# Performance work log

Hardware: AMD Instinct MI355X
Metric: run time of the kernel (lower is better)

Reference implementation:

```python
import jax, jax.numpy as jnp
import numpy as np

N = 100000
E = 800000

def elu(x):
    return jnp.where(x > 0, x, jnp.expm1(x))

def transformer_conv(x, src, dst, ea, Wq, bq, Wk, bk, Wv, bv, We, Ws, bs, heads, ch):
    # PyG TransformerConv (concat=True, root_weight=True, beta=False, eval so dropout off)
    n = x.shape[0]
    q = (x @ Wq + bq).reshape(n, heads, ch)
    k = (x @ Wk + bk).reshape(n, heads, ch)
    v = (x @ Wv + bv).reshape(n, heads, ch)
    e = (ea @ We).reshape(-1, heads, ch)            # [E,H,C], lin_edge has no bias
    kj = k[src] + e                                  # [E,H,C]
    logits = (q[dst] * kj).sum(-1) / jnp.sqrt(jnp.float32(ch))  # [E,H]
    # segment softmax over incoming edges of each dst node
    m = jax.ops.segment_max(logits, dst, num_segments=n)
    ex = jnp.exp(logits - m[dst])
    denom = jax.ops.segment_sum(ex, dst, num_segments=n)
    alpha = ex / denom[dst]                          # [E,H]
    msg = alpha[..., None] * (v[src] + e)            # [E,H,C]
    agg = jax.ops.segment_sum(msg, dst, num_segments=n).reshape(n, heads * ch)
    return agg + x @ Ws + bs                         # skip connection (lin_skip)

def setup_inputs() -> dict:
    key = jax.random.key(0)
    ks = jax.random.split(key, 32)
    def rn(k, shape, scale=0.1):
        return jax.random.normal(k, shape, dtype=jnp.float32) * scale
    d = {}
    d['x'] = jax.random.normal(ks[0], (N, 23), dtype=jnp.float32)
    d['edge_index'] = jax.random.randint(ks[1], (2, E), 0, N, dtype=jnp.int32)
    d['edge_attr'] = jax.random.normal(ks[2], (E, 7), dtype=jnp.float32)
    d['linA_w'] = rn(ks[3], (23, 23)); d['linA_b'] = jnp.zeros((23,), jnp.float32)
    d['linB_w'] = rn(ks[4], (23, 23)); d['linB_b'] = jnp.zeros((23,), jnp.float32)
    # conv1: in=23, heads=8, out=24 -> 192
    d['q1_w'] = rn(ks[5], (23, 192)); d['q1_b'] = jnp.zeros((192,), jnp.float32)
    d['k1_w'] = rn(ks[6], (23, 192)); d['k1_b'] = jnp.zeros((192,), jnp.float32)
    d['v1_w'] = rn(ks[7], (23, 192)); d['v1_b'] = jnp.zeros((192,), jnp.float32)
    d['e1_w'] = rn(ks[8], (7, 192))
    d['s1_w'] = rn(ks[9], (23, 192)); d['s1_b'] = jnp.zeros((192,), jnp.float32)
    # conv4: in=192, heads=8, out=8 -> 64
    d['q2_w'] = rn(ks[10], (192, 64)); d['q2_b'] = jnp.zeros((64,), jnp.float32)
    d['k2_w'] = rn(ks[11], (192, 64)); d['k2_b'] = jnp.zeros((64,), jnp.float32)
    d['v2_w'] = rn(ks[12], (192, 64)); d['v2_b'] = jnp.zeros((64,), jnp.float32)
    d['e2_w'] = rn(ks[13], (7, 64))
    d['s2_w'] = rn(ks[14], (192, 64)); d['s2_b'] = jnp.zeros((64,), jnp.float32)
    d['lin1_w'] = rn(ks[15], (64, 20)); d['lin1_b'] = jnp.zeros((20,), jnp.float32)
    d['lin2_w'] = rn(ks[16], (20, 1)); d['lin2_b'] = jnp.zeros((1,), jnp.float32)
    return d

def reference(x, edge_index, edge_attr,
              linA_w, linA_b, linB_w, linB_b,
              q1_w, q1_b, k1_w, k1_b, v1_w, v1_b, e1_w, s1_w, s1_b,
              q2_w, q2_b, k2_w, k2_b, v2_w, v2_b, e2_w, s2_w, s2_b,
              lin1_w, lin1_b, lin2_w, lin2_b):
    src, dst = edge_index[0], edge_index[1]
    h = elu(x @ linA_w + linA_b)
    h = elu(h @ linB_w + linB_b)
    h = transformer_conv(h, src, dst, edge_attr, q1_w, q1_b, k1_w, k1_b, v1_w, v1_b, e1_w, s1_w, s1_b, 8, 24)
    h = elu(h)
    h = transformer_conv(h, src, dst, edge_attr, q2_w, q2_b, k2_w, k2_b, v2_w, v2_b, e2_w, s2_w, s2_b, 8, 8)
    h = elu(h)
    h = elu(h @ lin1_w + lin1_b)
    return h @ lin2_w + lin2_b
```

## Files before the change

### kernel.cpp

```cpp
#include <hip/hip_runtime.h>
#include <math.h>


__device__ __forceinline__ float elu_f(float x) {
    return x > 0.f ? x : expm1f(x);
}


__global__ void mlp_kernel(const float* __restrict__ x,
                           const float* __restrict__ A, const float* __restrict__ ab,
                           const float* __restrict__ B, const float* __restrict__ bb,
                           float* __restrict__ out, int n) {
    __shared__ float sA[23 * 23], sB[23 * 23], sa[23], sb[23];
    for (int t = threadIdx.x; t < 23 * 23; t += blockDim.x) { sA[t] = A[t]; sB[t] = B[t]; }
    if (threadIdx.x < 23) { sa[threadIdx.x] = ab[threadIdx.x]; sb[threadIdx.x] = bb[threadIdx.x]; }
    __syncthreads();
    int i = blockIdx.x * blockDim.x + threadIdx.x;
    if (i >= n) return;
    float xi[23], h1[23];
    #pragma unroll
    for (int j = 0; j < 23; j++) xi[j] = x[(size_t)i * 23 + j];
    #pragma unroll
    for (int o = 0; o < 23; o++) {
        float acc = sa[o];
        #pragma unroll
        for (int j = 0; j < 23; j++) acc = fmaf(xi[j], sA[j * 23 + o], acc);
        h1[o] = elu_f(acc);
    }
    #pragma unroll
    for (int o = 0; o < 23; o++) {
        float acc = sb[o];
        #pragma unroll
        for (int j = 0; j < 23; j++) acc = fmaf(h1[j], sB[j * 23 + o], acc);
        out[(size_t)i * 23 + o] = elu_f(acc);
    }
}

__device__ __forceinline__ void store_val(int mode, int kvcpl, void* base, int stride,
                                          int g, int c, float val) {
    if (mode == 0) {
        ((float*)base)[(size_t)g * stride + c] = val;
    } else {
        int ln = c / kvcpl, slot = c - ln * kvcpl;
        size_t pos = (size_t)g * stride + (size_t)ln * (2 * kvcpl) + slot
                   + (mode == 2 ? kvcpl : 0);
        ((float*)base)[pos] = val;
    }
}

template<int IN, int Kc, int OUTW, int M, int TY, int KVCPL>
__global__ void proj_tiled_kernel(const float* __restrict__ in, int n,
    const float* __restrict__ W0, const float* __restrict__ b0, void* __restrict__ o0, int st0, int md0,
    const float* __restrict__ W1, const float* __restrict__ b1, void* __restrict__ o1, int st1, int md1,
    const float* __restrict__ W2, const float* __restrict__ b2, void* __restrict__ o2, int st2, int md2,
    const float* __restrict__ W3, const float* __restrict__ b3, void* __restrict__ o3, int st3, int md3) {
    constexpr int WTOT = M * OUTW;
    constexpr int CG   = WTOT / 8;
    constexpr int BN   = TY * 4;
    constexpr int SAW  = BN + 4;
    constexpr int NT   = CG * TY;
    static_assert(IN % Kc == 0, "Kc must divide IN");
    __shared__ float sA[Kc][SAW];
    __shared__ float sB[Kc][WTOT];

    const int tid = threadIdx.x;
    const int tx = tid % CG;
    const int ty = tid / CG;
    const int node0 = blockIdx.x * BN;

    const int colA = tx * 4;
    const int colB = WTOT / 2 + tx * 4;
    const int matA = colA / OUTW, ccA = colA % OUTW;
    const int matB = colB / OUTW, ccB = colB % OUTW;
    const float* bA = (matA == 0 ? b0 : matA == 1 ? b1 : matA == 2 ? b2 : b3);
    const float* bB = (matB == 0 ? b0 : matB == 1 ? b1 : matB == 2 ? b2 : b3);
    void* oA = (matA == 0 ? o0 : matA == 1 ? o1 : matA == 2 ? o2 : o3);
    void* oB = (matB == 0 ? o0 : matB == 1 ? o1 : matB == 2 ? o2 : o3);
    const int stA = (matA == 0 ? st0 : matA == 1 ? st1 : matA == 2 ? st2 : st3);
    const int stB = (matB == 0 ? st0 : matB == 1 ? st1 : matB == 2 ? st2 : st3);
    const int mdA = (matA == 0 ? md0 : matA == 1 ? md1 : matA == 2 ? md2 : md3);
    const int mdB = (matB == 0 ? md0 : matB == 1 ? md1 : matB == 2 ? md2 : md3);

    float acc[4][8];
    #pragma unroll
    for (int i = 0; i < 4; i++) {
        #pragma unroll
        for (int c = 0; c < 4; c++) { acc[i][c] = bA[ccA + c]; acc[i][4 + c] = bB[ccB + c]; }
    }

    for (int k0 = 0; k0 < IN; k0 += Kc) {
        for (int t = tid; t < Kc * BN; t += NT) {
            int j = t / BN, nn = t - j * BN;
            int g = node0 + nn;
            sA[j][nn] = (g < n) ? in[(size_t)g * IN + k0 + j] : 0.f;
        }
        for (int t = tid; t < Kc * WTOT; t += NT) {
            int j = t / WTOT, c = t - j * WTOT;
            int m = c / OUTW, cm = c - m * OUTW;
            const float* Wp = (m == 0 ? W0 : m == 1 ? W1 : m == 2 ? W2 : W3);
            sB[j][c] = Wp[(size_t)(k0 + j) * OUTW + cm];
        }
        __syncthreads();
        #pragma unroll 8
        for (int j = 0; j < Kc; j++) {
            float4 a  = *(const float4*)&sA[j][ty * 4];
            float4 v0 = *(const float4*)&sB[j][colA];
            float4 v1 = *(const float4*)&sB[j][colB];
            float av[4] = {a.x, a.y, a.z, a.w};
            float bv[8] = {v0.x, v0.y, v0.z, v0.w, v1.x, v1.y, v1.z, v1.w};
            #pragma unroll
            for (int i = 0; i < 4; i++)
                #pragma unroll
                for (int c = 0; c < 8; c++)
                    acc[i][c] = fmaf(av[i], bv[c], acc[i][c]);
        }
        __syncthreads();
    }

    #pragma unroll
    for (int i = 0; i < 4; i++) {
        int g = node0 + ty * 4 + i;
        if (g >= n) continue;
        #pragma unroll
        for (int c = 0; c < 4; c++) {
            store_val(mdA, KVCPL, oA, stA, g, ccA + c, acc[i][c]);
            store_val(mdB, KVCPL, oB, stB, g, ccB + c, acc[i][4 + c]);
        }
    }
}


__global__ void zero2_kernel(int* __restrict__ a, int* __restrict__ b, int n) {
    int i = blockIdx.x * blockDim.x + threadIdx.x;
    if (i < n) { a[i] = 0; b[i] = 0; }
}

__global__ void count_kernel(const int* __restrict__ dst, int* __restrict__ cnt, int nE) {
    int e = blockIdx.x * blockDim.x + threadIdx.x;
    if (e < nE) atomicAdd(&cnt[dst[e]], 1);
}

__global__ void scan_block_kernel(int* __restrict__ cnt, int* __restrict__ bsum, int n) {
    __shared__ int sdat[256];
    int i = blockIdx.x * 256 + threadIdx.x;
    int v = (i < n) ? cnt[i] : 0;
    sdat[threadIdx.x] = v;
    __syncthreads();
    for (int off = 1; off < 256; off <<= 1) {
        int t = (threadIdx.x >= (unsigned)off) ? sdat[threadIdx.x - off] : 0;
        __syncthreads();
        sdat[threadIdx.x] += t;
        __syncthreads();
    }
    if (i < n) cnt[i] = sdat[threadIdx.x] - v;
    if (threadIdx.x == 255) bsum[blockIdx.x] = sdat[255];
}

__global__ void scan_bsum_kernel(int* __restrict__ bsum, int nb) {
    __shared__ int s[1024];
    int i = threadIdx.x;
    int v = (i < nb) ? bsum[i] : 0;
    s[i] = v;
    __syncthreads();
    for (int off = 1; off < 1024; off <<= 1) {
        int t = (i >= off) ? s[i - off] : 0;
        __syncthreads();
        s[i] += t;
        __syncthreads();
    }
    if (i < nb) bsum[i] = s[i] - v;
}

__global__ void finalize_rp_kernel(const int* __restrict__ cnt, const int* __restrict__ bsum,
                                   int* __restrict__ rp, int n, int nE) {
    int i = blockIdx.x * blockDim.x + threadIdx.x;
    if (i < n) rp[i] = cnt[i] + bsum[i >> 8];
    if (i == n) rp[n] = nE;
}

__global__ void scatter_kernel(const int* __restrict__ src, const int* __restrict__ dst,
                               const int* __restrict__ rp, int* __restrict__ cur,
                               int* __restrict__ srcS, int* __restrict__ eidS, int nE) {
    int e = blockIdx.x * blockDim.x + threadIdx.x;
    if (e >= nE) return;
    int d = dst[e];
    int pos = rp[d] + atomicAdd(&cur[d], 1);
    srcS[pos] = src[e];
    eidS[pos] = e;
}

template<int IN, int C, bool QMAT, bool DOELU>
__global__ void conv_fused_kernel(const float* __restrict__ feat,
                                  const float* __restrict__ Wq, const float* __restrict__ qb,
                                  const float* __restrict__ kv,
                                  const float* __restrict__ qmat,
                                  const float* __restrict__ ea, const float* __restrict__ We,
                                  const int* __restrict__ rp, const int* __restrict__ srcS,
                                  const int* __restrict__ eidS,
                                  float* __restrict__ out, int n, float scale) {
    constexpr int HC = 8 * C;
    constexpr int CPL = HC / 64;
    constexpr int KVROW = 2 * HC;
    const int lane = threadIdx.x & 63;
    const int d = blockIdx.x * (blockDim.x >> 6) + (threadIdx.x >> 6);
    if (d >= n) return;
    const int ch0 = lane * CPL;

    float we[7][CPL];
    #pragma unroll
    for (int j = 0; j < 7; j++)
        #pragma unroll
        for (int c = 0; c < CPL; c++) we[j][c] = We[j * HC + ch0 + c];

    float* op = out + (size_t)d * HC + ch0;
    float sk[CPL], q[CPL];
    #pragma unroll
    for (int c = 0; c < CPL; c++) sk[c] = op[c];
    if constexpr (QMAT) {
        const float* qp = qmat + (size_t)d * HC + ch0;
        #pragma unroll
        for (int c = 0; c < CPL; c++) q[c] = qp[c];
    } else {
        #pragma unroll
        for (int c = 0; c < CPL; c++) q[c] = qb[ch0 + c];
        const float* fd = feat + (size_t)d * IN;
        for (int j = 0; j < IN; j++) {
            float f = fd[j];
            #pragma unroll
            for (int c = 0; c < CPL; c++)
                q[c] = fmaf(f, Wq[(size_t)j * HC + ch0 + c], q[c]);
        }
    }

    float m = -INFINITY, l = 0.f, acc[CPL];
    #pragma unroll
    for (int c = 0; c < CPL; c++) acc[c] = 0.f;

    const int p0 = rp[d], p1 = rp[d + 1];
    if (p0 < p1) {
        auto loadkv = [&](int s, float* kc, float* vc) {
            const float* pb = kv + (size_t)s * KVROW + lane * (2 * CPL);
            if constexpr (CPL == 3) {
                float2 a = *(const float2*)(pb + 0);
                float2 b = *(const float2*)(pb + 2);
                float2 c = *(const float2*)(pb + 4);
                kc[0] = a.x; kc[1] = a.y; kc[2] = b.x;
                vc[0] = b.y; vc[1] = c.x; vc[2] = c.y;
            } else {
                float2 a = *(const float2*)pb;
                kc[0] = a.x; vc[0] = a.y;
            }
        };
        float kc[CPL], vc[CPL], ev[7];
        loadkv(srcS[p0], kc, vc);
        {
            const float* e0 = ea + (size_t)eidS[p0] * 7;
            #pragma unroll
            for (int j = 0; j < 7; j++) ev[j] = e0[j];
        }

        for (int p = p0; p < p1; p++) {
            float kn[CPL], vn[CPL], evn[7];
            if (p + 1 < p1) {
                loadkv(srcS[p + 1], kn, vn);
                const float* e1 = ea + (size_t)eidS[p + 1] * 7;
                #pragma unroll
                for (int j = 0; j < 7; j++) evn[j] = e1[j];
            }
            float part = 0.f, vv[CPL];
            #pragma unroll
            for (int c = 0; c < CPL; c++) {
                float ec = 0.f;
                #pragma unroll
                for (int j = 0; j < 7; j++) ec = fmaf(ev[j], we[j][c], ec);
                part = fmaf(q[c], kc[c] + ec, part);
                vv[c] = vc[c] + ec;
            }
            part += __shfl_xor(part, 1);
            part += __shfl_xor(part, 2);
            part += __shfl_xor(part, 4);
            float z = part * scale;
            float mn = fmaxf(m, z);
            float rs = expf(m - mn);
            float pw = expf(z - mn);
            l = l * rs + pw;
            #pragma unroll
            for (int c = 0; c < CPL; c++) acc[c] = fmaf(acc[c], rs, pw * vv[c]);
            m = mn;
            #pragma unroll
            for (int c = 0; c < CPL; c++) { kc[c] = kn[c]; vc[c] = vn[c]; }
            #pragma unroll
            for (int j = 0; j < 7; j++) ev[j] = evn[j];
        }
    }
    float invl = (l > 0.f) ? 1.f / l : 0.f;
    #pragma unroll
    for (int c = 0; c < CPL; c++) {
        float r = sk[c] + acc[c] * invl;
        op[c] = DOELU ? elu_f(r) : r;
    }
}

__global__ void head_kernel(const float* __restrict__ h, const float* __restrict__ W1,
                            const float* __restrict__ b1, const float* __restrict__ W2,
                            const float* __restrict__ b2, float* __restrict__ out, int n) {
    __shared__ float sW1[64 * 20], sb1[20], sW2[20], sb2;
    for (int t = threadIdx.x; t < 64 * 20; t += blockDim.x) sW1[t] = W1[t];
    if (threadIdx.x < 20) { sb1[threadIdx.x] = b1[threadIdx.x]; sW2[threadIdx.x] = W2[threadIdx.x]; }
    if (threadIdx.x == 0) sb2 = b2[0];
    __syncthreads();
    int i = blockIdx.x * blockDim.x + threadIdx.x;
    if (i >= n) return;
    float hv[64];
    const float* hp = h + (size_t)i * 64;
    #pragma unroll
    for (int j = 0; j < 64; j++) hv[j] = elu_f(hp[j]);
    float acc2 = sb2;
    for (int o = 0; o < 20; o++) {
        float a = sb1[o];
        #pragma unroll
        for (int j = 0; j < 64; j++) a = fmaf(hv[j], sW1[j * 20 + o], a);
        acc2 = fmaf(elu_f(a), sW2[o], acc2);
    }
    out[i] = acc2;
}

__global__ void zero_out_kernel(float* __restrict__ out, int n) {
    int i = blockIdx.x * blockDim.x + threadIdx.x;
    if (i < n) out[i] = 0.f;
}


extern "C" void kernel_launch(void* const* d_in, const int* in_sizes, int n_in,
                              void* d_out, int out_size, void* d_ws, size_t ws_size,
                              hipStream_t stream) {
    const float* x   = (const float*)d_in[0];
    const int*   ei  = (const int*)d_in[1];
    const float* ea  = (const float*)d_in[2];
    const float* Aw  = (const float*)d_in[3];
    const float* Ab  = (const float*)d_in[4];
    const float* Bw  = (const float*)d_in[5];
    const float* Bb  = (const float*)d_in[6];
    const float* q1w = (const float*)d_in[7];  const float* q1b = (const float*)d_in[8];
    const float* k1w = (const float*)d_in[9];  const float* k1b = (const float*)d_in[10];
    const float* v1w = (const float*)d_in[11]; const float* v1b = (const float*)d_in[12];
    const float* e1w = (const float*)d_in[13];
    const float* s1w = (const float*)d_in[14]; const float* s1b = (const float*)d_in[15];
    const float* q2w = (const float*)d_in[16]; const float* q2b = (const float*)d_in[17];
    const float* k2w = (const float*)d_in[18]; const float* k2b = (const float*)d_in[19];
    const float* v2w = (const float*)d_in[20]; const float* v2b = (const float*)d_in[21];
    const float* e2w = (const float*)d_in[22];
    const float* s2w = (const float*)d_in[23]; const float* s2b = (const float*)d_in[24];
    const float* l1w = (const float*)d_in[25]; const float* l1b = (const float*)d_in[26];
    const float* l2w = (const float*)d_in[27]; const float* l2b = (const float*)d_in[28];

    const int n  = in_sizes[0] / 23;
    const int nE = in_sizes[1] / 2;
    const int* src = ei;
    const int* dst = ei + nE;
    float* out = (float*)d_out;
    const int B = 256;
    const int nb = (n + 255) / 256;

    size_t fl_h1 = ((size_t)n * 23 + 3) & ~(size_t)3;
    size_t fl_o1 = (size_t)n * 192;
    size_t fl_kv = (size_t)n * 384;
    size_t ints_total = ((size_t)n + 1) + n + n + 1024 + (size_t)nE + (size_t)nE;
    size_t need_bytes = (fl_h1 + fl_o1 + fl_kv) * 4 + ints_total * 4;

    if (ws_size < need_bytes || nb > 1024) {
        zero_out_kernel<<<(out_size + B - 1) / B, B, 0, stream>>>(out, out_size);
        return;
    }

    float* ws = (float*)d_ws;
    size_t off = 0;
    float* h1    = ws + off; off += fl_h1;
    float* o1    = ws + off; off += fl_o1;
    float* kvreg = ws + off; off += fl_kv;
    int* ip = (int*)(ws + off);
    int* rp   = ip; ip += (size_t)n + 1;
    int* cnt  = ip; ip += n;
    int* cur  = ip; ip += n;
    int* bsum = ip; ip += 1024;
    int* srcS = ip; ip += nE;
    int* eidS = ip; ip += nE;

    float* kv1   = kvreg;
    float* kv2   = kvreg;
    float* q2buf = kvreg + (size_t)n * 128;
    float* o2    = kvreg + (size_t)n * 192;

    const float sc1 = 1.0f / sqrtf(24.0f);
    const float sc2 = 1.0f / sqrtf(8.0f);
    const float* np = nullptr;
    void* npv = nullptr;

    zero2_kernel<<<(n + B - 1) / B, B, 0, stream>>>(cnt, cur, n);
    count_kernel<<<(nE + B - 1) / B, B, 0, stream>>>(dst, cnt, nE);
    scan_block_kernel<<<nb, 256, 0, stream>>>(cnt, bsum, n);
    scan_bsum_kernel<<<1, 1024, 0, stream>>>(bsum, nb);
    finalize_rp_kernel<<<(n + 1 + B - 1) / B, B, 0, stream>>>(cnt, bsum, rp, n, nE);
    scatter_kernel<<<(nE + B - 1) / B, B, 0, stream>>>(src, dst, rp, cur, srcS, eidS, nE);

    mlp_kernel<<<(n + B - 1) / B, B, 0, stream>>>(x, Aw, Ab, Bw, Bb, h1, n);

    const int gproj = (n + 31) / 32;

    proj_tiled_kernel<23, 23, 192, 3, 8, 3><<<gproj, 576, 0, stream>>>(
        h1, n,
        k1w, k1b, (void*)kv1, 384, 1,
        v1w, v1b, (void*)kv1, 384, 2,
        s1w, s1b, (void*)o1, 192, 0,
        np, np, npv, 0, 0);
    conv_fused_kernel<23, 24, false, true><<<(n + 3) / 4, 256, 0, stream>>>(
        h1, q1w, q1b, kv1, np, ea, e1w, rp, srcS, eidS, o1, n, sc1);

    proj_tiled_kernel<192, 32, 64, 4, 8, 1><<<gproj, 256, 0, stream>>>(
        o1, n,
        q2w, q2b, (void*)q2buf, 64, 0,
        k2w, k2b, (void*)kv2, 128, 1,
        v2w, v2b, (void*)kv2, 128, 2,
        s2w, s2b, (void*)o2, 64, 0);
    conv_fused_kernel<192, 8, true, false><<<(n + 3) / 4, 256, 0, stream>>>(
        o1, q2w, q2b, kv2, q2buf, ea, e2w, rp, srcS, eidS, o2, n, sc2);

    head_kernel<<<(n + B - 1) / B, B, 0, stream>>>(o2, l1w, l1b, l2w, l2b, out, n);
}
```

Before: 1.155 ms.

## Process two destination nodes per wavefront and vectorize projection stores

```diff
diff --git a/kernel.cpp b/kernel.cpp
--- a/kernel.cpp
+++ b/kernel.cpp
@@ -36,30 +36,22 @@
     }
 }
 
-__device__ __forceinline__ void store_val(int mode, int kvcpl, void* base, int stride,
-                                          int g, int c, float val) {
-    if (mode == 0) {
-        ((float*)base)[(size_t)g * stride + c] = val;
-    } else {
-        int ln = c / kvcpl, slot = c - ln * kvcpl;
-        size_t pos = (size_t)g * stride + (size_t)ln * (2 * kvcpl) + slot
-                   + (mode == 2 ? kvcpl : 0);
-        ((float*)base)[pos] = val;
-    }
-}
-
-template<int IN, int Kc, int OUTW, int M, int TY, int KVCPL>
+template<int IN, int Kc, int OUTW, int M, int TY, int KM, int VM>
 __global__ void proj_tiled_kernel(const float* __restrict__ in, int n,
-    const float* __restrict__ W0, const float* __restrict__ b0, void* __restrict__ o0, int st0, int md0,
-    const float* __restrict__ W1, const float* __restrict__ b1, void* __restrict__ o1, int st1, int md1,
-    const float* __restrict__ W2, const float* __restrict__ b2, void* __restrict__ o2, int st2, int md2,
-    const float* __restrict__ W3, const float* __restrict__ b3, void* __restrict__ o3, int st3, int md3) {
+    const float* __restrict__ W0, const float* __restrict__ b0,
+    const float* __restrict__ W1, const float* __restrict__ b1,
+    const float* __restrict__ W2, const float* __restrict__ b2,
+    const float* __restrict__ W3, const float* __restrict__ b3,
+    float* __restrict__ kvout,
+    float* __restrict__ r0, float* __restrict__ r1,
+    float* __restrict__ r2, float* __restrict__ r3) {
     constexpr int WTOT = M * OUTW;
     constexpr int CG   = WTOT / 8;
     constexpr int BN   = TY * 4;
     constexpr int SAW  = BN + 4;
     constexpr int NT   = CG * TY;
-    static_assert(IN % Kc == 0, "Kc must divide IN");
+    constexpr int PT   = OUTW / 4;
+    static_assert(IN % Kc == 0, "Kc divides IN");
     __shared__ float sA[Kc][SAW];
     __shared__ float sB[Kc][WTOT];
 
@@ -68,18 +60,30 @@
     const int ty = tid / CG;
     const int node0 = blockIdx.x * BN;
 
-    const int colA = tx * 4;
-    const int colB = WTOT / 2 + tx * 4;
+    int colA, colB; bool pairkv; int chan0 = 0;
+    if (tx < PT) {
+        pairkv = true; chan0 = 4 * tx;
+        colA = KM * OUTW + chan0;
+        colB = VM * OUTW + chan0;
+    } else {
+        pairkv = false;
+        int u = 8 * (tx - PT);
+        auto remap = [&](int uu) {
+            int ri = uu / OUTW, cc = uu - ri * OUTW;
+            int cnt = 0, mat = 0;
+            for (int mm = 0; mm < M; mm++) {
+                if (mm == KM || mm == VM) continue;
+                if (cnt == ri) { mat = mm; break; }
+                cnt++;
+            }
+            return mat * OUTW + cc;
+        };
+        colA = remap(u); colB = remap(u + 4);
+    }
     const int matA = colA / OUTW, ccA = colA % OUTW;
     const int matB = colB / OUTW, ccB = colB % OUTW;
     const float* bA = (matA == 0 ? b0 : matA == 1 ? b1 : matA == 2 ? b2 : b3);
     const float* bB = (matB == 0 ? b0 : matB == 1 ? b1 : matB == 2 ? b2 : b3);
-    void* oA = (matA == 0 ? o0 : matA == 1 ? o1 : matA == 2 ? o2 : o3);
-    void* oB = (matB == 0 ? o0 : matB == 1 ? o1 : matB == 2 ? o2 : o3);
-    const int stA = (matA == 0 ? st0 : matA == 1 ? st1 : matA == 2 ? st2 : st3);
-    const int stB = (matB == 0 ? st0 : matB == 1 ? st1 : matB == 2 ? st2 : st3);
-    const int mdA = (matA == 0 ? md0 : matA == 1 ? md1 : matA == 2 ? md2 : md3);
-    const int mdB = (matB == 0 ? md0 : matB == 1 ? md1 : matB == 2 ? md2 : md3);
 
     float acc[4][8];
     #pragma unroll
@@ -121,10 +125,15 @@
     for (int i = 0; i < 4; i++) {
         int g = node0 + ty * 4 + i;
         if (g >= n) continue;
-        #pragma unroll
-        for (int c = 0; c < 4; c++) {
-            store_val(mdA, KVCPL, oA, stA, g, ccA + c, acc[i][c]);
-            store_val(mdB, KVCPL, oB, stB, g, ccB + c, acc[i][4 + c]);
+        if (pairkv) {
+            float* kp = kvout + (size_t)g * (2 * OUTW) + 2 * chan0;
+            *(float4*)(kp + 0) = make_float4(acc[i][0], acc[i][4], acc[i][1], acc[i][5]);
+            *(float4*)(kp + 4) = make_float4(acc[i][2], acc[i][6], acc[i][3], acc[i][7]);
+        } else {
+            float* rA = (matA == 0 ? r0 : matA == 1 ? r1 : matA == 2 ? r2 : r3);
+            float* rB = (matB == 0 ? r0 : matB == 1 ? r1 : matB == 2 ? r2 : r3);
+            *(float4*)(rA + (size_t)g * OUTW + ccA) = make_float4(acc[i][0], acc[i][1], acc[i][2], acc[i][3]);
+            *(float4*)(rB + (size_t)g * OUTW + ccB) = make_float4(acc[i][4], acc[i][5], acc[i][6], acc[i][7]);
         }
     }
 }
@@ -190,20 +199,22 @@
 }
 
 template<int IN, int C, bool QMAT, bool DOELU>
-__global__ void conv_fused_kernel(const float* __restrict__ feat,
-                                  const float* __restrict__ Wq, const float* __restrict__ qb,
-                                  const float* __restrict__ kv,
-                                  const float* __restrict__ qmat,
-                                  const float* __restrict__ ea, const float* __restrict__ We,
-                                  const int* __restrict__ rp, const int* __restrict__ srcS,
-                                  const int* __restrict__ eidS,
-                                  float* __restrict__ out, int n, float scale) {
+__global__ void conv_fused2_kernel(const float* __restrict__ feat,
+                                   const float* __restrict__ Wq, const float* __restrict__ qb,
+                                   const float* __restrict__ kv,
+                                   const float* __restrict__ qmat,
+                                   const float* __restrict__ ea, const float* __restrict__ We,
+                                   const int* __restrict__ rp, const int* __restrict__ srcS,
+                                   const int* __restrict__ eidS,
+                                   float* __restrict__ out, int n, float scale) {
     constexpr int HC = 8 * C;
     constexpr int CPL = HC / 64;
     constexpr int KVROW = 2 * HC;
     const int lane = threadIdx.x & 63;
-    const int d = blockIdx.x * (blockDim.x >> 6) + (threadIdx.x >> 6);
-    if (d >= n) return;
+    const int w = blockIdx.x * (blockDim.x >> 6) + (threadIdx.x >> 6);
+    const int d0 = 2 * w;
+    if (d0 >= n) return;
+    const bool has1 = (d0 + 1) < n;
     const int ch0 = lane * CPL;
 
     float we[7][CPL];
@@ -212,92 +223,123 @@
         #pragma unroll
         for (int c = 0; c < CPL; c++) we[j][c] = We[j * HC + ch0 + c];
 
-    float* op = out + (size_t)d * HC + ch0;
-    float sk[CPL], q[CPL];
-    #pragma unroll
-    for (int c = 0; c < CPL; c++) sk[c] = op[c];
+    float* op0 = out + (size_t)d0 * HC + ch0;
+    float* op1 = op0 + HC;
+    float sk0[CPL], sk1[CPL], q0[CPL], q1[CPL];
+    #pragma unroll
+    for (int c = 0; c < CPL; c++) sk0[c] = op0[c];
+    if (has1) {
+        #pragma unroll
+        for (int c = 0; c < CPL; c++) sk1[c] = op1[c];
+    }
     if constexpr (QMAT) {
-        const float* qp = qmat + (size_t)d * HC + ch0;
-        #pragma unroll
-        for (int c = 0; c < CPL; c++) q[c] = qp[c];
+        const float* qp0 = qmat + (size_t)d0 * HC + ch0;
+        #pragma unroll
+        for (int c = 0; c < CPL; c++) q0[c] = qp0[c];
+        if (has1) {
+            const float* qp1 = qp0 + HC;
+            #pragma unroll
+            for (int c = 0; c < CPL; c++) q1[c] = qp1[c];
+        }
     } else {
         #pragma unroll
-        for (int c = 0; c < CPL; c++) q[c] = qb[ch0 + c];
-        const float* fd = feat + (size_t)d * IN;
+        for (int c = 0; c < CPL; c++) { q0[c] = qb[ch0 + c]; q1[c] = qb[ch0 + c]; }
+        const float* fd0 = feat + (size_t)d0 * IN;
+        const float* fd1 = fd0 + IN;
         for (int j = 0; j < IN; j++) {
-            float f = fd[j];
-            #pragma unroll
-            for (int c = 0; c < CPL; c++)
-                q[c] = fmaf(f, Wq[(size_t)j * HC + ch0 + c], q[c]);
-        }
-    }
-
-    float m = -INFINITY, l = 0.f, acc[CPL];
-    #pragma unroll
-    for (int c = 0; c < CPL; c++) acc[c] = 0.f;
-
-    const int p0 = rp[d], p1 = rp[d + 1];
-    if (p0 < p1) {
-        auto loadkv = [&](int s, float* kc, float* vc) {
-            const float* pb = kv + (size_t)s * KVROW + lane * (2 * CPL);
-            if constexpr (CPL == 3) {
-                float2 a = *(const float2*)(pb + 0);
-                float2 b = *(const float2*)(pb + 2);
-                float2 c = *(const float2*)(pb + 4);
-                kc[0] = a.x; kc[1] = a.y; kc[2] = b.x;
-                vc[0] = b.y; vc[1] = c.x; vc[2] = c.y;
-            } else {
-                float2 a = *(const float2*)pb;
-                kc[0] = a.x; vc[0] = a.y;
+            float f0 = fd0[j];
+            float f1 = has1 ? fd1[j] : 0.f;
+            #pragma unroll
+            for (int c = 0; c < CPL; c++) {
+                float wv = Wq[(size_t)j * HC + ch0 + c];
+                q0[c] = fmaf(f0, wv, q0[c]);
+                q1[c] = fmaf(f1, wv, q1[c]);
             }
-        };
-        float kc[CPL], vc[CPL], ev[7];
-        loadkv(srcS[p0], kc, vc);
-        {
-            const float* e0 = ea + (size_t)eidS[p0] * 7;
-            #pragma unroll
-            for (int j = 0; j < 7; j++) ev[j] = e0[j];
-        }
-
-        for (int p = p0; p < p1; p++) {
-            float kn[CPL], vn[CPL], evn[7];
-            if (p + 1 < p1) {
-                loadkv(srcS[p + 1], kn, vn);
-                const float* e1 = ea + (size_t)eidS[p + 1] * 7;
-                #pragma unroll
-                for (int j = 0; j < 7; j++) evn[j] = e1[j];
-            }
-            float part = 0.f, vv[CPL];
-            #pragma unroll
-            for (int c = 0; c < CPL; c++) {
-                float ec = 0.f;
-                #pragma unroll
-                for (int j = 0; j < 7; j++) ec = fmaf(ev[j], we[j][c], ec);
-                part = fmaf(q[c], kc[c] + ec, part);
-                vv[c] = vc[c] + ec;
-            }
-            part += __shfl_xor(part, 1);
-            part += __shfl_xor(part, 2);
-            part += __shfl_xor(part, 4);
-            float z = part * scale;
-            float mn = fmaxf(m, z);
-            float rs = expf(m - mn);
-            float pw = expf(z - mn);
-            l = l * rs + pw;
-            #pragma unroll
-            for (int c = 0; c < CPL; c++) acc[c] = fmaf(acc[c], rs, pw * vv[c]);
-            m = mn;
-            #pragma unroll
-            for (int c = 0; c < CPL; c++) { kc[c] = kn[c]; vc[c] = vn[c]; }
-            #pragma unroll
-            for (int j = 0; j < 7; j++) ev[j] = evn[j];
-        }
-    }
-    float invl = (l > 0.f) ? 1.f / l : 0.f;
+        }
+    }
+
+    auto loadEdge = [&](int p, float* kc, float* vc, float* ev) {
+        int s = srcS[p], eid = eidS[p];
+        const float* pb = kv + (size_t)s * KVROW + 2 * ch0;
+        #pragma unroll
+        for (int c = 0; c < CPL; c++) {
+            float2 t = *(const float2*)(pb + 2 * c);
+            kc[c] = t.x; vc[c] = t.y;
+        }
+        const float* ep = ea + (size_t)eid * 7;
+        #pragma unroll
+        for (int j = 0; j < 7; j++) ev[j] = ep[j];
+    };
+    auto step = [&](const float* qv, float& m, float& l, float* accv,
+                    const float* kc, const float* vc, const float* ev) {
+        float part = 0.f, vv[CPL];
+        #pragma unroll
+        for (int c = 0; c < CPL; c++) {
+            float ec = 0.f;
+            #pragma unroll
+            for (int j = 0; j < 7; j++) ec = fmaf(ev[j], we[j][c], ec);
+            part = fmaf(qv[c], kc[c] + ec, part);
+            vv[c] = vc[c] + ec;
+        }
+        part += __shfl_xor(part, 1);
+        part += __shfl_xor(part, 2);
+        part += __shfl_xor(part, 4);
+        float z = part * scale;
+        float mn = fmaxf(m, z);
+        float rs = expf(m - mn);
+        float pw = expf(z - mn);
+        l = l * rs + pw;
+        #pragma unroll
+        for (int c = 0; c < CPL; c++) accv[c] = fmaf(accv[c], rs, pw * vv[c]);
+        m = mn;
+    };
+
+    float m0 = -INFINITY, l0 = 0.f, acc0[CPL];
+    float m1 = -INFINITY, l1 = 0.f, acc1[CPL];
+    #pragma unroll
+    for (int c = 0; c < CPL; c++) { acc0[c] = 0.f; acc1[c] = 0.f; }
+
+    int a = rp[d0], aE = rp[d0 + 1];
+    int b = has1 ? aE : 0, bE = has1 ? rp[d0 + 2] : 0;
+
+    float kA[CPL], vA[CPL], eA[7], kB[CPL], vB[CPL], eB[7];
+    if (a < aE) loadEdge(a, kA, vA, eA);
+    if (b < bE) loadEdge(b, kB, vB, eB);
+
+    while (a < aE || b < bE) {
+        float kA2[CPL], vA2[CPL], eA2[7], kB2[CPL], vB2[CPL], eB2[7];
+        bool nA = (a + 1) < aE, nB = (b + 1) < bE;
+        if (nA) loadEdge(a + 1, kA2, vA2, eA2);
+        if (nB) loadEdge(b + 1, kB2, vB2, eB2);
+        if (a < aE) { step(q0, m0, l0, acc0, kA, vA, eA); a++; }
+        if (b < bE) { step(q1, m1, l1, acc1, kB, vB, eB); b++; }
+        if (nA) {
+            #pragma unroll
+            for (int c = 0; c < CPL; c++) { kA[c] = kA2[c]; vA[c] = vA2[c]; }
+            #pragma unroll
+            for (int j = 0; j < 7; j++) eA[j] = eA2[j];
+        }
+        if (nB) {
+            #pragma unroll
+            for (int c = 0; c < CPL; c++) { kB[c] = kB2[c]; vB[c] = vB2[c]; }
+            #pragma unroll
+            for (int j = 0; j < 7; j++) eB[j] = eB2[j];
+        }
+    }
+
+    float il0 = (l0 > 0.f) ? 1.f / l0 : 0.f;
     #pragma unroll
     for (int c = 0; c < CPL; c++) {
-        float r = sk[c] + acc[c] * invl;
-        op[c] = DOELU ? elu_f(r) : r;
+        float r = sk0[c] + acc0[c] * il0;
+        op0[c] = DOELU ? elu_f(r) : r;
+    }
+    if (has1) {
+        float il1 = (l1 > 0.f) ? 1.f / l1 : 0.f;
+        #pragma unroll
+        for (int c = 0; c < CPL; c++) {
+            float r = sk1[c] + acc1[c] * il1;
+            op1[c] = DOELU ? elu_f(r) : r;
+        }
     }
 }
 
@@ -394,7 +436,7 @@
     const float sc1 = 1.0f / sqrtf(24.0f);
     const float sc2 = 1.0f / sqrtf(8.0f);
     const float* np = nullptr;
-    void* npv = nullptr;
+    float* npw = nullptr;
 
     zero2_kernel<<<(n + B - 1) / B, B, 0, stream>>>(cnt, cur, n);
     count_kernel<<<(nE + B - 1) / B, B, 0, stream>>>(dst, cnt, nE);
@@ -405,24 +447,16 @@
 
     mlp_kernel<<<(n + B - 1) / B, B, 0, stream>>>(x, Aw, Ab, Bw, Bb, h1, n);
 
-    const int gproj = (n + 31) / 32;
-
-    proj_tiled_kernel<23, 23, 192, 3, 8, 3><<<gproj, 576, 0, stream>>>(
-        h1, n,
-        k1w, k1b, (void*)kv1, 384, 1,
-        v1w, v1b, (void*)kv1, 384, 2,
-        s1w, s1b, (void*)o1, 192, 0,
-        np, np, npv, 0, 0);
-    conv_fused_kernel<23, 24, false, true><<<(n + 3) / 4, 256, 0, stream>>>(
+    proj_tiled_kernel<23, 23, 192, 3, 8, 0, 1><<<(n + 31) / 32, 576, 0, stream>>>(
+        h1, n, k1w, k1b, v1w, v1b, s1w, s1b, np, np,
+        kv1, npw, npw, o1, npw);
+    conv_fused2_kernel<23, 24, false, true><<<(n + 7) / 8, 256, 0, stream>>>(
         h1, q1w, q1b, kv1, np, ea, e1w, rp, srcS, eidS, o1, n, sc1);
 
-    proj_tiled_kernel<192, 32, 64, 4, 8, 1><<<gproj, 256, 0, stream>>>(
-        o1, n,
-        q2w, q2b, (void*)q2buf, 64, 0,
-        k2w, k2b, (void*)kv2, 128, 1,
-        v2w, v2b, (void*)kv2, 128, 2,
-        s2w, s2b, (void*)o2, 64, 0);
-    conv_fused_kernel<192, 8, true, false><<<(n + 3) / 4, 256, 0, stream>>>(
+    proj_tiled_kernel<192, 32, 64, 4, 16, 1, 2><<<(n + 63) / 64, 512, 0, stream>>>(
+        o1, n, q2w, q2b, k2w, k2b, v2w, v2b, s2w, s2b,
+        kv2, q2buf, npw, npw, o2);
+    conv_fused2_kernel<192, 8, true, false><<<(n + 7) / 8, 256, 0, stream>>>(
         o1, q2w, q2b, kv2, q2buf, ea, e2w, rp, srcS, eidS, o2, n, sc2);
 
     head_kernel<<<(n + B - 1) / B, B, 0, stream>>>(o2, l1w, l1b, l2w, l2b, out, n);
```

After: 1.779 ms. 1.54x slower.
